# Kernel tuning notes

Hardware: AMD Instinct MI355X
Metric: run time of the kernel (lower is better)

## Reference

```python
import jax, jax.numpy as jnp
import numpy as np

NORM_S = 3.0  # normalize_scale, learn_scale=False
NUM_CLASSES = 32


def setup_inputs() -> dict:
    key = jax.random.key(0)
    k1, k2 = jax.random.split(key)
    x = jax.random.normal(k1, (512, 128), dtype=jnp.float32)
    labels = jax.random.randint(k2, (512,), 0, NUM_CLASSES, dtype=jnp.int64)
    return {"x": x, "labels": labels}


def reference(x, labels):
    # L2-normalize rows and scale (MyTripletLoss.forward)
    f = NORM_S * x / jnp.linalg.norm(x, axis=1, keepdims=True)
    # pairwise squared distances, clamped at 0 (pairwise_distances)
    sq = jnp.sum(f * f, axis=1)
    D = jnp.clip(sq[:, None] + sq[None, :] - 2.0 * (f @ f.T), 0.0, None)  # [N,N]
    N = x.shape[0]
    # triplet_type == 0: valid triplet (i,j,k) iff i!=j, l_i==l_j, l_i!=l_k
    same = (labels[:, None] == labels[None, :]) & (~jnp.eye(N, dtype=bool))  # [i,j]
    diff = labels[:, None] != labels[None, :]                                # [i,k]
    mask = same[:, :, None] & diff[:, None, :]                               # [i,j,k]
    # DBL loss: log(1 + exp(D_ij - D_ik)) = softplus
    lt = jax.nn.softplus(D[:, :, None] - D[:, None, :])                      # [i,j,k]
    triplet_count = jnp.sum(mask).astype(lt.dtype)
    loss = jnp.sum(jnp.where(mask, lt, 0.0)) / triplet_count
    return loss.reshape(1)
```

## Files before the change

kernel.cpp:

```cpp
#include <hip/hip_runtime.h>
#include <math.h>

#define N 512
#define DIM 128
#define TR 128
#define PADS 132
#define BT 512


__global__ void __launch_bounds__(BT) triplet_kernel(const float* __restrict__ x,
                                                     const int* __restrict__ labels,
                                                     float* __restrict__ sums,
                                                     float* __restrict__ cnts) {
    __shared__ float xt[TR * PADS];
    __shared__ int   lab[N];
    __shared__ float dotv[N];
    __shared__ float ssqv[N];
    __shared__ float sameD[N];
    __shared__ float diffD[N];
    __shared__ float red[BT / 64];
    __shared__ int   nsame, ndiff;

    int i = blockIdx.x;
    int t = threadIdx.x;

    lab[t] = labels[t];
    if (t == 0) { nsame = 0; ndiff = 0; }

    int quart = t & 3;
    int jloc  = t >> 2;
    int dbase = quart * 32;

    float4 bx[8];
    {
        const float4* b = (const float4*)(x + i * DIM + dbase);
        #pragma unroll
        for (int q = 0; q < 8; ++q) bx[q] = b[q];
    }
    __syncthreads();

    for (int tile = 0; tile < N / TR; ++tile) {
        int base = tile * TR;
        const float4* src = (const float4*)(x + base * DIM);
        #pragma unroll
        for (int k = 0; k < (TR * DIM / 4) / BT; ++k) {
            int e  = t + k * BT;
            int r  = e >> 5;
            int c4 = e & 31;
            float4 v = src[e];
            *((float4*)(xt + r * PADS + 4 * c4)) = v;
        }
        __syncthreads();

        const float4* a = (const float4*)(xt + jloc * PADS + dbase);
        float d0 = 0.0f, d1 = 0.0f, s0 = 0.0f, s1 = 0.0f;
        #pragma unroll
        for (int q = 0; q < 8; q += 2) {
            float4 a0 = a[q + 0];
            float4 a1 = a[q + 1];
            d0 += a0.x * bx[q].x + a0.y * bx[q].y + a0.z * bx[q].z + a0.w * bx[q].w;
            d1 += a1.x * bx[q + 1].x + a1.y * bx[q + 1].y + a1.z * bx[q + 1].z + a1.w * bx[q + 1].w;
            s0 += a0.x * a0.x + a0.y * a0.y + a0.z * a0.z + a0.w * a0.w;
            s1 += a1.x * a1.x + a1.y * a1.y + a1.z * a1.z + a1.w * a1.w;
        }
        float dsum = d0 + d1;
        float ssum = s0 + s1;
        dsum += __shfl_xor(dsum, 1, 64);
        dsum += __shfl_xor(dsum, 2, 64);
        ssum += __shfl_xor(ssum, 1, 64);
        ssum += __shfl_xor(ssum, 2, 64);
        if (quart == 0) {
            dotv[base + jloc] = dsum;
            ssqv[base + jloc] = ssum;
        }
        __syncthreads();
    }

    {
        float rni = rsqrtf(ssqv[i]);
        int j = t;
        float D = 18.0f * fmaxf(0.0f, 1.0f - dotv[j] * rsqrtf(ssqv[j]) * rni);
        int li = lab[i];
        if (lab[j] == li) {
            if (j != i) { int p = atomicAdd(&nsame, 1); sameD[p] = D; }
        } else {
            int p = atomicAdd(&ndiff, 1); diffD[p] = D;
        }
    }
    __syncthreads();

    int ns = nsame, nd = ndiff;
    float ek = (t < nd) ? __expf(-diffD[t]) : 0.0f;
    float lsum = 0.0f;
    float snext = (ns > 0) ? sameD[0] : 0.0f;
    for (int js = 0; js < ns; ++js) {
        float ds = snext;
        snext = sameD[js + 1];
        float es = __expf(ds);
        lsum += __logf(1.0f + es * ek);
    }

    #pragma unroll
    for (int off = 32; off > 0; off >>= 1) lsum += __shfl_xor(lsum, off, 64);
    if ((t & 63) == 0) red[t >> 6] = lsum;
    __syncthreads();
    if (t == 0) {
        float s = 0.0f;
        #pragma unroll
        for (int w = 0; w < BT / 64; ++w) s += red[w];
        sums[i] = s;
        cnts[i] = (float)(ns * nd);
    }
}

__global__ void __launch_bounds__(256) finalize_kernel(const float* __restrict__ sums,
                                                       const float* __restrict__ cnts,
                                                       float* __restrict__ out) {
    __shared__ float2 red[256];
    int t = threadIdx.x;
    float2 v;
    v.x = sums[t] + sums[t + 256];
    v.y = cnts[t] + cnts[t + 256];
    red[t] = v;
    __syncthreads();
    #pragma unroll
    for (int s = 128; s > 0; s >>= 1) {
        if (t < s) {
            red[t].x += red[t + s].x;
            red[t].y += red[t + s].y;
        }
        __syncthreads();
    }
    if (t == 0) out[0] = red[0].x / red[0].y;
}

extern "C" void kernel_launch(void* const* d_in, const int* in_sizes, int n_in,
                              void* d_out, int out_size, void* d_ws, size_t ws_size,
                              hipStream_t stream) {
    const float* x      = (const float*)d_in[0];
    const int*   labels = (const int*)d_in[1];
    float*       out    = (float*)d_out;

    float* sums = (float*)d_ws;
    float* cnts = sums + N;

    triplet_kernel<<<N, BT, 0, stream>>>(x, labels, sums, cnts);
    finalize_kernel<<<1, 256, 0, stream>>>(sums, cnts, out);
}
```

Measured before the change: 71.11 us.

## Split into tiled Gram-matrix kernel and per-row loss kernel with last-block reduction

```diff
diff --git a/kernel.cpp b/kernel.cpp
--- a/kernel.cpp
+++ b/kernel.cpp
@@ -3,101 +3,122 @@
 
 #define N 512
 #define DIM 128
-#define TR 128
+#define TT 32
 #define PADS 132
-#define BT 512
+#define GB (N / TT)
 
 
-__global__ void __launch_bounds__(BT) triplet_kernel(const float* __restrict__ x,
-                                                     const int* __restrict__ labels,
-                                                     float* __restrict__ sums,
-                                                     float* __restrict__ cnts) {
-    __shared__ float xt[TR * PADS];
-    __shared__ int   lab[N];
-    __shared__ float dotv[N];
-    __shared__ float ssqv[N];
-    __shared__ float sameD[N];
-    __shared__ float diffD[N];
-    __shared__ float red[BT / 64];
-    __shared__ int   nsame, ndiff;
+__global__ void __launch_bounds__(256) gram_kernel(const float* __restrict__ x,
+                                                   float* __restrict__ D,
+                                                   int* __restrict__ done) {
+    __shared__ float xi[TT * PADS];
+    __shared__ float xj[TT * PADS];
+    __shared__ float rnA[TT];
+    __shared__ float rnB[TT];
 
-    int i = blockIdx.x;
+    int bi = blockIdx.y, bj = blockIdx.x;
     int t = threadIdx.x;
+    if (bi == 0 && bj == 0 && t == 0) *done = 0;
 
-    lab[t] = labels[t];
-    if (t == 0) { nsame = 0; ndiff = 0; }
-
-    int quart = t & 3;
-    int jloc  = t >> 2;
-    int dbase = quart * 32;
-
-    float4 bx[8];
-    {
-        const float4* b = (const float4*)(x + i * DIM + dbase);
-        #pragma unroll
-        for (int q = 0; q < 8; ++q) bx[q] = b[q];
+    const float4* srcA = (const float4*)(x + bi * TT * DIM);
+    const float4* srcB = (const float4*)(x + bj * TT * DIM);
+    #pragma unroll
+    for (int k = 0; k < (TT * DIM / 4) / 256; ++k) {
+        int e = t + k * 256;
+        int r = e >> 5, c4 = e & 31;
+        *((float4*)(xi + r * PADS + 4 * c4)) = srcA[e];
+        *((float4*)(xj + r * PADS + 4 * c4)) = srcB[e];
     }
     __syncthreads();
 
-    for (int tile = 0; tile < N / TR; ++tile) {
-        int base = tile * TR;
-        const float4* src = (const float4*)(x + base * DIM);
-        #pragma unroll
-        for (int k = 0; k < (TR * DIM / 4) / BT; ++k) {
-            int e  = t + k * BT;
-            int r  = e >> 5;
-            int c4 = e & 31;
-            float4 v = src[e];
-            *((float4*)(xt + r * PADS + 4 * c4)) = v;
-        }
-        __syncthreads();
-
-        const float4* a = (const float4*)(xt + jloc * PADS + dbase);
-        float d0 = 0.0f, d1 = 0.0f, s0 = 0.0f, s1 = 0.0f;
+    {
+        int quart = t & 3, r = t >> 2;
+        const float* base = (r < TT) ? (xi + r * PADS) : (xj + (r - TT) * PADS);
+        const float4* a = (const float4*)(base + quart * 32);
+        float s0 = 0.0f, s1 = 0.0f;
         #pragma unroll
         for (int q = 0; q < 8; q += 2) {
-            float4 a0 = a[q + 0];
-            float4 a1 = a[q + 1];
-            d0 += a0.x * bx[q].x + a0.y * bx[q].y + a0.z * bx[q].z + a0.w * bx[q].w;
-            d1 += a1.x * bx[q + 1].x + a1.y * bx[q + 1].y + a1.z * bx[q + 1].z + a1.w * bx[q + 1].w;
+            float4 a0 = a[q], a1 = a[q + 1];
             s0 += a0.x * a0.x + a0.y * a0.y + a0.z * a0.z + a0.w * a0.w;
             s1 += a1.x * a1.x + a1.y * a1.y + a1.z * a1.z + a1.w * a1.w;
         }
-        float dsum = d0 + d1;
-        float ssum = s0 + s1;
-        dsum += __shfl_xor(dsum, 1, 64);
-        dsum += __shfl_xor(dsum, 2, 64);
-        ssum += __shfl_xor(ssum, 1, 64);
-        ssum += __shfl_xor(ssum, 2, 64);
+        float ss = s0 + s1;
+        ss += __shfl_xor(ss, 1, 64);
+        ss += __shfl_xor(ss, 2, 64);
         if (quart == 0) {
-            dotv[base + jloc] = dsum;
-            ssqv[base + jloc] = ssum;
-        }
-        __syncthreads();
-    }
-
-    {
-        float rni = rsqrtf(ssqv[i]);
-        int j = t;
-        float D = 18.0f * fmaxf(0.0f, 1.0f - dotv[j] * rsqrtf(ssqv[j]) * rni);
-        int li = lab[i];
-        if (lab[j] == li) {
-            if (j != i) { int p = atomicAdd(&nsame, 1); sameD[p] = D; }
-        } else {
-            int p = atomicAdd(&ndiff, 1); diffD[p] = D;
+            if (r < TT) rnA[r] = rsqrtf(ss);
+            else        rnB[r - TT] = rsqrtf(ss);
         }
     }
     __syncthreads();
 
+    int tx = t & 15, ty = t >> 4;
+    int i0 = 2 * ty, i1 = i0 + 1, j0 = 2 * tx, j1 = j0 + 1;
+    float acc00 = 0.0f, acc01 = 0.0f, acc10 = 0.0f, acc11 = 0.0f;
+    const float4* A0 = (const float4*)(xi + i0 * PADS);
+    const float4* A1 = (const float4*)(xi + i1 * PADS);
+    const float4* B0 = (const float4*)(xj + j0 * PADS);
+    const float4* B1 = (const float4*)(xj + j1 * PADS);
+    #pragma unroll 8
+    for (int k4 = 0; k4 < DIM / 4; ++k4) {
+        float4 a0 = A0[k4], a1 = A1[k4], b0 = B0[k4], b1 = B1[k4];
+        acc00 += a0.x * b0.x + a0.y * b0.y + a0.z * b0.z + a0.w * b0.w;
+        acc01 += a0.x * b1.x + a0.y * b1.y + a0.z * b1.z + a0.w * b1.w;
+        acc10 += a1.x * b0.x + a1.y * b0.y + a1.z * b0.z + a1.w * b0.w;
+        acc11 += a1.x * b1.x + a1.y * b1.y + a1.z * b1.z + a1.w * b1.w;
+    }
+    float ri0 = rnA[i0], ri1 = rnA[i1], rj0 = rnB[j0], rj1 = rnB[j1];
+    int gi0 = bi * TT + i0, gi1 = bi * TT + i1, gj = bj * TT + j0;
+    float2 r0, r1;
+    r0.x = 18.0f * fmaxf(0.0f, 1.0f - acc00 * ri0 * rj0);
+    r0.y = 18.0f * fmaxf(0.0f, 1.0f - acc01 * ri0 * rj1);
+    r1.x = 18.0f * fmaxf(0.0f, 1.0f - acc10 * ri1 * rj0);
+    r1.y = 18.0f * fmaxf(0.0f, 1.0f - acc11 * ri1 * rj1);
+    *((float2*)(D + gi0 * N + gj)) = r0;
+    *((float2*)(D + gi1 * N + gj)) = r1;
+}
+
+__global__ void __launch_bounds__(256) loss_kernel(const float* __restrict__ Dm,
+                                                   const int* __restrict__ labels,
+                                                   float* __restrict__ sums,
+                                                   float* __restrict__ cnts,
+                                                   int* __restrict__ done,
+                                                   float* __restrict__ out) {
+    __shared__ int   lab[N];
+    __shared__ float sameD[N];
+    __shared__ float diffD[N];
+    __shared__ float red[4];
+    __shared__ float rs[4], rc[4];
+    __shared__ int   nsame, ndiff, lastFlag;
+
+    int i = blockIdx.x, t = threadIdx.x;
+    lab[t]       = labels[t];
+    lab[t + 256] = labels[t + 256];
+    if (t == 0) { nsame = 0; ndiff = 0; }
+    float d0 = Dm[i * N + t];
+    float d1 = Dm[i * N + t + 256];
+    __syncthreads();
+
+    int li = lab[i];
+    {
+        int j = t;
+        if (lab[j] == li) {
+            if (j != i) { int p = atomicAdd(&nsame, 1); sameD[p] = d0; }
+        } else { int p = atomicAdd(&ndiff, 1); diffD[p] = d0; }
+        j = t + 256;
+        if (lab[j] == li) {
+            if (j != i) { int p = atomicAdd(&nsame, 1); sameD[p] = d1; }
+        } else { int p = atomicAdd(&ndiff, 1); diffD[p] = d1; }
+    }
+    __syncthreads();
+
     int ns = nsame, nd = ndiff;
-    float ek = (t < nd) ? __expf(-diffD[t]) : 0.0f;
+    float ek0 = (t < nd)       ? __expf(-diffD[t])       : 0.0f;
+    float ek1 = (t + 256 < nd) ? __expf(-diffD[t + 256]) : 0.0f;
     float lsum = 0.0f;
-    float snext = (ns > 0) ? sameD[0] : 0.0f;
     for (int js = 0; js < ns; ++js) {
-        float ds = snext;
-        snext = sameD[js + 1];
-        float es = __expf(ds);
-        lsum += __logf(1.0f + es * ek);
+        float es = __expf(sameD[js]);
+        lsum += __logf(1.0f + es * ek0) + __logf(1.0f + es * ek1);
     }
 
     #pragma unroll
@@ -105,33 +126,27 @@
     if ((t & 63) == 0) red[t >> 6] = lsum;
     __syncthreads();
     if (t == 0) {
-        float s = 0.0f;
-        #pragma unroll
-        for (int w = 0; w < BT / 64; ++w) s += red[w];
-        sums[i] = s;
+        sums[i] = red[0] + red[1] + red[2] + red[3];
         cnts[i] = (float)(ns * nd);
     }
-}
-
-__global__ void __launch_bounds__(256) finalize_kernel(const float* __restrict__ sums,
-                                                       const float* __restrict__ cnts,
-                                                       float* __restrict__ out) {
-    __shared__ float2 red[256];
-    int t = threadIdx.x;
-    float2 v;
-    v.x = sums[t] + sums[t + 256];
-    v.y = cnts[t] + cnts[t + 256];
-    red[t] = v;
+    __threadfence();
+    if (t == 0) lastFlag = (atomicAdd(done, 1) == N - 1) ? 1 : 0;
     __syncthreads();
-    #pragma unroll
-    for (int s = 128; s > 0; s >>= 1) {
-        if (t < s) {
-            red[t].x += red[t + s].x;
-            red[t].y += red[t + s].y;
+    if (lastFlag) {
+        __threadfence();
+        float s = sums[t] + sums[t + 256];
+        float c = cnts[t] + cnts[t + 256];
+        #pragma unroll
+        for (int off = 32; off > 0; off >>= 1) {
+            s += __shfl_xor(s, off, 64);
+            c += __shfl_xor(c, off, 64);
         }
+        if ((t & 63) == 0) { rs[t >> 6] = s; rc[t >> 6] = c; }
         __syncthreads();
+        if (t == 0)
+            out[0] = (rs[0] + rs[1] + rs[2] + rs[3]) /
+                     (rc[0] + rc[1] + rc[2] + rc[3]);
     }
-    if (t == 0) out[0] = red[0].x / red[0].y;
 }
 
 extern "C" void kernel_launch(void* const* d_in, const int* in_sizes, int n_in,
@@ -141,9 +156,11 @@
     const int*   labels = (const int*)d_in[1];
     float*       out    = (float*)d_out;
 
-    float* sums = (float*)d_ws;
+    float* Dm   = (float*)d_ws;
+    float* sums = Dm + N * N;
     float* cnts = sums + N;
+    int*   done = (int*)(cnts + N);
 
-    triplet_kernel<<<N, BT, 0, stream>>>(x, labels, sums, cnts);
-    finalize_kernel<<<1, 256, 0, stream>>>(sums, cnts, out);
+    gram_kernel<<<dim3(GB, GB), 256, 0, stream>>>(x, Dm, done);
+    loss_kernel<<<N, 256, 0, stream>>>(Dm, labels, sums, cnts, done, out);
 }
```

After: 102.3 us. 43.8% more time.
